# Kernel tuning notes

Hardware: AMD Instinct MI355X
Metric: run time of the kernel (lower is better)

The kernel has to match this reference:

```python
import jax, jax.numpy as jnp
import numpy as np

B, N, S = 256, 512, 32
D_ENT, D_KEY, D_IN, D_FUNC, D_TYPE, H = 256, 32, 1024, 256, 259, 32


def _init_linear(k, out_d, in_d):
    kw, kb = jax.random.split(k)
    bound = 1.0 / np.sqrt(in_d)
    W = jax.random.uniform(kw, (out_d, in_d), minval=-bound, maxval=bound, dtype=jnp.float32)
    b = jax.random.uniform(kb, (out_d,), minval=-bound, maxval=bound, dtype=jnp.float32)
    return W, b


def setup_inputs() -> dict:
    key = jax.random.key(0)
    ks = jax.random.split(key, 16)
    inp = {
        "embedding": jax.random.normal(ks[0], (B, D_IN), jnp.float32),
        "available_unit_type_mask": (jax.random.uniform(ks[1], (B, D_TYPE)) < 0.5).astype(jnp.float32),
        "available_units_mask": jnp.ones((B, N), jnp.float32),
        "entity_embedding": jax.random.normal(ks[2], (B, N, D_ENT), jnp.float32),
        "selected_units": jax.random.randint(ks[3], (B, S), 0, N, dtype=jnp.int32),
        "end_embedding": jax.random.uniform(ks[4], (1, D_KEY), minval=-1.0, maxval=1.0, dtype=jnp.float32) / np.sqrt(D_KEY),
    }
    inp["W_key"], inp["b_key"] = _init_linear(ks[5], D_KEY, D_ENT)
    inp["W_func"], inp["b_func"] = _init_linear(ks[6], D_FUNC, D_TYPE)
    inp["W_fc1"], inp["b_fc1"] = _init_linear(ks[7], D_FUNC, D_IN)
    inp["W_fc2"], inp["b_fc2"] = _init_linear(ks[8], D_KEY, D_FUNC)
    inp["W_embed"], inp["b_embed"] = _init_linear(ks[9], D_IN, D_KEY)
    inp["W_ih"], inp["b_ih"] = _init_linear(ks[10], 4 * H, D_KEY)
    inp["W_hh"], inp["b_hh"] = _init_linear(ks[11], 4 * H, H)
    return inp


def reference(embedding, available_unit_type_mask, available_units_mask, entity_embedding,
              selected_units, end_embedding, W_key, b_key, W_func, b_func, W_fc1, b_fc1,
              W_fc2, b_fc2, W_embed, b_embed, W_ih, b_ih, W_hh, b_hh):
    Bv, Nv, _ = entity_embedding.shape
    Sv = selected_units.shape[1]
    # keys for each entity + end-flag embedding appended -> [B, N+1, key_dim]
    key_t = jnp.einsum('bnd,kd->bnk', entity_embedding, W_key) + b_key
    end = jnp.broadcast_to(end_embedding[None, :, :], (Bv, 1, end_embedding.shape[1]))
    pad_key = jnp.concatenate([key_t, end], axis=1)
    # mask: entities + end flag; teacher-forced selected positions forced to 1
    mask0 = jnp.concatenate([available_units_mask, jnp.ones((Bv, 1), available_units_mask.dtype)], axis=1)
    mask0 = mask0.at[jnp.arange(Bv)[:, None], selected_units].set(1.0)
    func_embed = jax.nn.relu(available_unit_type_mask @ W_func.T + b_func)
    inv_n = 1.0 / jnp.float32(Nv)  # split_entity_num = end_flag_index = num_units
    bidx = jnp.arange(Bv)
    # per-step selected index (dummy 0 on the final end-flag step) and validity
    sel_seq = jnp.concatenate([selected_units.T, jnp.zeros((1, Bv), selected_units.dtype)], axis=0)
    valid_seq = jnp.concatenate([jnp.ones((Sv, Bv), jnp.float32), jnp.zeros((1, Bv), jnp.float32)], axis=0)

    def step(carry, xs):
        emb, h, c, mask = carry
        sel, valid = xs
        # query = fc2(relu(fc1(emb) + func_embed))
        x = jax.nn.relu(emb @ W_fc1.T + b_fc1 + func_embed) @ W_fc2.T + b_fc2
        # one LSTM step
        gates = x @ W_ih.T + b_ih + h @ W_hh.T + b_hh
        i_g, f_g, g_g, o_g = jnp.split(gates, 4, axis=1)
        c = jax.nn.sigmoid(f_g) * c + jax.nn.sigmoid(i_g) * jnp.tanh(g_g)
        h = jax.nn.sigmoid(o_g) * jnp.tanh(c)
        # masked dot-product over keys -> logits [B, N+1]
        q = jnp.einsum('bk,bnk->bn', h, pad_key) - (1.0 - mask) * 1e9
        # mark selected unit unavailable for subsequent steps
        mask = mask.at[bidx, sel].set(jnp.where(valid > 0, 0.0, mask[bidx, sel]))
        # one-hot gather of selected key, averaged, fed back into embedding
        emb_sel = pad_key[bidx, sel] * inv_n
        emb = emb + (emb_sel @ W_embed.T + b_embed) * valid[:, None]
        return (emb, h, c, mask), q

    h0 = jnp.zeros((Bv, W_hh.shape[1]), jnp.float32)
    c0 = jnp.zeros_like(h0)
    (emb, _, _, _), logits = jax.lax.scan(step, (embedding, h0, c0, mask0), (sel_seq, valid_seq))
    logits = jnp.transpose(logits, (1, 0, 2))  # [B, S+1, N+1]
    return logits, emb
```

## Files before the change

kernel.cpp:

```cpp
#include <hip/hip_runtime.h>
#include <math.h>

#define BB_ 256
#define NN_ 512
#define SS_ 32
#define NP1 513
#define SP1 33
#define D_IN 1024
#define D_TYPE 259
#define INV_N (1.0f/512.0f)

#define N_ACT 256
#define COMB_BASE 256
#define N_COMB 32
#define END_BID 288
#define KEY_BASE 289
#define N_KEY 2048
#define FRONT_GRID (KEY_BASE + N_KEY)

typedef short s16x4 __attribute__((ext_vector_type(4)));
typedef short s16x8 __attribute__((ext_vector_type(8)));
typedef float f32x4 __attribute__((ext_vector_type(4)));

#if defined(__has_builtin)
#if __has_builtin(__builtin_amdgcn_rcpf)
#define FRCP(x) __builtin_amdgcn_rcpf(x)
#else
#define FRCP(x) (1.0f / (x))
#endif
#else
#define FRCP(x) (1.0f / (x))
#endif

__device__ __forceinline__ float fsig(float x) { return FRCP(1.0f + __expf(-x)); }
__device__ __forceinline__ float ftanh(float x) { return fmaf(-2.0f, FRCP(1.0f + __expf(2.0f * x)), 1.0f); }
__device__ __forceinline__ short f2bf(float f) {
    unsigned u = __float_as_uint(f);
    unsigned r = (u + 0x7FFFu + ((u >> 16) & 1u)) >> 16;
    return (short)r;
}
__device__ __forceinline__ float bf2f(short s) {
    unsigned u = ((unsigned)(unsigned short)s) << 16;
    return __uint_as_float(u);
}

__global__ __launch_bounds__(256) void front_kernel(
    const float* __restrict__ ent, const float* __restrict__ Wk,
    const float* __restrict__ bk, const float* __restrict__ endv,
    const float* __restrict__ Wemb, const float* __restrict__ bemb,
    const float* __restrict__ Wfc1, const float* __restrict__ emb0,
    const float* __restrict__ bfc1, const float* __restrict__ atm,
    const float* __restrict__ Wf, const float* __restrict__ bf,
    short* __restrict__ pkbf, float* __restrict__ WcombT,
    float* __restrict__ cbv, float* __restrict__ act_pre)
{
    __shared__ __align__(128) char u_raw[65536];
    short* a_st   = (short*)u_raw;
    float* wemb_s = (float*)(u_raw + 18688);
    float* a_lds  = (float*)u_raw;
    float* w_lds  = (float*)(u_raw + 16640);

    const int tid = threadIdx.x;
    const int bid = blockIdx.x;
    const int lane = tid & 63, w = tid >> 6;
    const int nl = lane & 15, q = lane >> 4;

    if (bid >= KEY_BASE) {
        float* kb = (float*)u_raw;
        const size_t rowbase = (size_t)(bid - KEY_BASE) * 64;

#define KSTAGE(kc_) do {                                                          \
        _Pragma("unroll")                                                         \
        for (int p_ = 0; p_ < 4; p_++) {                                          \
            int flat_ = p_ * 256 + tid;                                           \
            int row_ = flat_ >> 4, u_ = flat_ & 15;                               \
            int gf4_ = (u_ & 8) | ((u_ ^ row_) & 7);                              \
            const float* src_ = ent + (((rowbase + (size_t)row_) << 8)            \
                                       + (kc_) * 64 + gf4_ * 4);                  \
            char* dst_ = u_raw + (kc_) * 16384 + ((p_ << 8) + (w << 6)) * 16;     \
            __builtin_amdgcn_global_load_lds(                                     \
                (const __attribute__((address_space(1))) void*)src_,              \
                (__attribute__((address_space(3))) void*)dst_, 16, 0, 0);         \
        }                                                                         \
    } while (0)

        KSTAGE(0);
        KSTAGE(1);
        KSTAGE(2);
        KSTAGE(3);

        s16x8 bfr[8][2];
#pragma unroll
        for (int s = 0; s < 8; s++)
#pragma unroll
            for (int t = 0; t < 2; t++) {
                const float* src = Wk + (size_t)(t * 16 + nl) * 256 + s * 32 + q * 8;
                float4 v0 = *(const float4*)(src);
                float4 v1 = *(const float4*)(src + 4);
                s16x8 bv;
                bv[0] = f2bf(v0.x); bv[1] = f2bf(v0.y); bv[2] = f2bf(v0.z); bv[3] = f2bf(v0.w);
                bv[4] = f2bf(v1.x); bv[5] = f2bf(v1.y); bv[6] = f2bf(v1.z); bv[7] = f2bf(v1.w);
                bfr[s][t] = bv;
            }

        f32x4 acc[2];
        acc[0] = (f32x4)0.0f; acc[1] = (f32x4)0.0f;

        const int rl = w * 16 + nl;
        const int rx = rl & 7;

#define KWAIT(n_) do {                                                            \
        asm volatile("s_waitcnt vmcnt(" #n_ ")" ::: "memory");                    \
        __builtin_amdgcn_s_barrier();                                             \
        asm volatile("" ::: "memory");                                            \
    } while (0)
#define KCOMPUTE(kc_) do {                                                        \
        const float* kbc = kb + (kc_) * 4096;                                     \
        _Pragma("unroll")                                                         \
        for (int ks = 0; ks < 2; ks++) {                                          \
            int s0 = ks * 8 + ((q * 2) ^ rx);                                     \
            int s1 = ks * 8 + ((q * 2 + 1) ^ rx);                                 \
            f32x4 a0 = *(const f32x4*)&kbc[rl * 64 + s0 * 4];                     \
            f32x4 a1 = *(const f32x4*)&kbc[rl * 64 + s1 * 4];                     \
            s16x8 af;                                                             \
            af[0] = f2bf(a0[0]); af[1] = f2bf(a0[1]);                             \
            af[2] = f2bf(a0[2]); af[3] = f2bf(a0[3]);                             \
            af[4] = f2bf(a1[0]); af[5] = f2bf(a1[1]);                             \
            af[6] = f2bf(a1[2]); af[7] = f2bf(a1[3]);                             \
            acc[0] = __builtin_amdgcn_mfma_f32_16x16x32_bf16(                     \
                af, bfr[(kc_) * 2 + ks][0], acc[0], 0, 0, 0);                     \
            acc[1] = __builtin_amdgcn_mfma_f32_16x16x32_bf16(                     \
                af, bfr[(kc_) * 2 + ks][1], acc[1], 0, 0, 0);                     \
        }                                                                         \
    } while (0)

        KWAIT(12); KCOMPUTE(0);
        KWAIT(8);  KCOMPUTE(1);
        KWAIT(4);  KCOMPUTE(2);
        KWAIT(0);  KCOMPUTE(3);

#undef KCOMPUTE
#undef KWAIT
#undef KSTAGE

        float bkv0 = bk[nl], bkv1 = bk[16 + nl];
#pragma unroll
        for (int t = 0; t < 2; t++)
#pragma unroll
            for (int r = 0; r < 4; r++) {
                int rowg = (int)rowbase + w * 16 + q * 4 + r;
                int b = rowg >> 9, n = rowg & 511;
                pkbf[((size_t)b * NP1 + n) * 32 + t * 16 + nl] =
                    f2bf(acc[t][r] + (t ? bkv1 : bkv0));
            }
    } else if (bid < N_ACT) {
        const int idx = bid;
        const int jt = idx & 15, bt = idx >> 4;
        const int bb = tid >> 4, jj = tid & 15;

#pragma unroll 4
        for (int r = 0; r < 16; r++) {
            a_lds[r * 260 + tid] = atm[(size_t)(bt * 16 + r) * D_TYPE + tid];
            w_lds[r * 260 + tid] = Wf[(size_t)(jt * 16 + r) * D_TYPE + tid];
            if (tid < 3) {
                a_lds[r * 260 + 256 + tid] = atm[(size_t)(bt * 16 + r) * D_TYPE + 256 + tid];
                w_lds[r * 260 + 256 + tid] = Wf[(size_t)(jt * 16 + r) * D_TYPE + 256 + tid];
            }
        }
        __syncthreads();
        float accf;
        {
            float f0 = 0.0f, f1 = 0.0f, f2 = 0.0f, f3 = 0.0f;
            const float4* ap = (const float4*)&a_lds[bb * 260];
            const float4* wp = (const float4*)&w_lds[jj * 260];
#pragma unroll 8
            for (int i4 = 0; i4 < 64; i4++) {
                float4 a = ap[i4]; float4 wv = wp[i4];
                f0 = fmaf(a.x, wv.x, f0); f1 = fmaf(a.y, wv.y, f1);
                f2 = fmaf(a.z, wv.z, f2); f3 = fmaf(a.w, wv.w, f3);
            }
            accf = (f0 + f1) + (f2 + f3);
            for (int i = 256; i < 259; i++) accf = fmaf(a_lds[bb * 260 + i], w_lds[jj * 260 + i], accf);
        }
        float c0 = 0.0f, c1 = 0.0f, c2 = 0.0f, c3 = 0.0f;
        for (int c = 0; c < 4; c++) {
            __syncthreads();
#pragma unroll
            for (int p = 0; p < 4; p++) {
                int l4 = p * 256 + tid;
                int r = l4 >> 6, k4 = l4 & 63;
                *(float4*)&a_lds[r * 260 + k4 * 4] =
                    *(const float4*)(emb0 + (size_t)(bt * 16 + r) * D_IN + c * 256 + k4 * 4);
                *(float4*)&w_lds[r * 260 + k4 * 4] =
                    *(const float4*)(Wfc1 + (size_t)(jt * 16 + r) * D_IN + c * 256 + k4 * 4);
            }
            __syncthreads();
#pragma unroll 8
            for (int k4 = 0; k4 < 64; k4++) {
                float4 a = *(const float4*)&a_lds[bb * 260 + k4 * 4];
                float4 wv = *(const float4*)&w_lds[jj * 260 + k4 * 4];
                c0 = fmaf(a.x, wv.x, c0); c1 = fmaf(a.y, wv.y, c1);
                c2 = fmaf(a.z, wv.z, c2); c3 = fmaf(a.w, wv.w, c3);
            }
        }
        float acc = (c0 + c1) + (c2 + c3);
        const int b = bt * 16 + bb, j = jt * 16 + jj;
        act_pre[b * 256 + j] = acc + bfc1[j] + fmaxf(accf + bf[j], 0.0f);
    } else if (bid < END_BID) {
        const int cb = bid - COMB_BASE;
        const int kc = cb >> 1;
        const int m0 = cb & 1;

#pragma unroll
        for (int p = 0; p < 8; p++) {
            int flat = p * 256 + tid;
            int row = flat >> 4;
            int f4 = flat & 15;
            float4 v = *(const float4*)(Wfc1 + (size_t)(m0 * 128 + row) * D_IN + kc * 64 + f4 * 4);
            s16x4 sv;
            sv[0] = f2bf(v.x); sv[1] = f2bf(v.y); sv[2] = f2bf(v.z); sv[3] = f2bf(v.w);
            *(s16x4*)&a_st[row * 72 + f4 * 4] = sv;
        }
        {
            int r = tid >> 2, c0 = tid & 3;
#pragma unroll
            for (int cc = 0; cc < 9; cc++) {
                int col = c0 + cc * 4;
                if (col < 33) {
                    float v = (col < 32) ? Wemb[(size_t)(kc * 64 + r) * 32 + col]
                                         : bemb[kc * 64 + r];
                    wemb_s[r * 33 + col] = v;
                }
            }
        }
        __syncthreads();

        f32x4 acc[2][3];
#pragma unroll
        for (int mt = 0; mt < 2; mt++)
#pragma unroll
            for (int t = 0; t < 3; t++) acc[mt][t] = (f32x4)0.0f;

#pragma unroll
        for (int ks = 0; ks < 2; ks++) {
            s16x8 bv[3];
#pragma unroll
            for (int t = 0; t < 3; t++) {
                int n = t * 16 + nl;
#pragma unroll
                for (int jj = 0; jj < 8; jj++) {
                    float v = (n < 33) ? wemb_s[(ks * 32 + q * 8 + jj) * 33 + n] : 0.0f;
                    bv[t][jj] = f2bf(v);
                }
            }
#pragma unroll
            for (int mt = 0; mt < 2; mt++) {
                s16x8 af = *(const s16x8*)&a_st[(w * 32 + mt * 16 + nl) * 72 + ks * 32 + q * 8];
#pragma unroll
                for (int t = 0; t < 3; t++)
                    acc[mt][t] = __builtin_amdgcn_mfma_f32_16x16x32_bf16(af, bv[t], acc[mt][t], 0, 0, 0);
            }
        }
#pragma unroll
        for (int mt = 0; mt < 2; mt++)
#pragma unroll
            for (int t = 0; t < 3; t++)
#pragma unroll
                for (int r = 0; r < 4; r++) {
                    int j = m0 * 128 + w * 32 + mt * 16 + q * 4 + r;
                    int n = t * 16 + nl;
                    if (n < 32) atomicAdd(&WcombT[j * 32 + n], acc[mt][t][r]);
                    else if (n == 32) atomicAdd(&cbv[j], acc[mt][t][r]);
                }
    } else {
        const int k = tid & 31, b0 = tid >> 5;
        short evk = f2bf(endv[k]);
        for (int b = b0; b < BB_; b += 8)
            pkbf[((size_t)b * NP1 + 512) * 32 + k] = evk;
    }
}

__global__ __launch_bounds__(512, 1) void back_kernel(
    const short* __restrict__ pkbf, const float* __restrict__ act_pre0,
    const int* __restrict__ sel, const float* __restrict__ avail,
    const float* __restrict__ Wfc2, const float* __restrict__ bfc2,
    const float* __restrict__ Wih, const float* __restrict__ bih,
    const float* __restrict__ bhh, const float* __restrict__ Whh,
    const float* __restrict__ WcombT, const float* __restrict__ cbv,
    const float* __restrict__ emb0, const float* __restrict__ Wemb,
    const float* __restrict__ bemb,
    float* __restrict__ logits, float* __restrict__ emb_out)
{
    __shared__ float S[19204];
    __shared__ int sel_l[SS_];
    float* rap_l  = S;
    float* red_l  = S + 8580;
    float* x_l    = S + 17028;
    float* cumE_l = S + 18084;
    float* ssel_l = S + 19140;
    float* xg_l   = S;
    float* h_all  = S + 4224;
    float* m0_l   = S + 8580;
    int*   tf_l   = (int*)(S + 9093);

    const int tid = threadIdx.x;
    const int b = blockIdx.x;
    const int lane = tid & 63, w = tid >> 6;
    const int nl = lane & 15, q = lane >> 4;

    if (tid < SS_) sel_l[tid] = sel[b * SS_ + tid];

    {
        const int k = tid & 31, sq = (tid >> 5) & 7;
        const int sq4 = sq * 4;
        int s0 = sel[b * SS_ + sq4 + 0];
        int s1 = sel[b * SS_ + sq4 + 1];
        int s2 = sel[b * SS_ + sq4 + 2];
        int s3 = sel[b * SS_ + sq4 + 3];
        float v0 = bf2f(pkbf[((size_t)b * NP1 + s0) * 32 + k]) * INV_N;
        float v1 = bf2f(pkbf[((size_t)b * NP1 + s1) * 32 + k]) * INV_N;
        float v2 = bf2f(pkbf[((size_t)b * NP1 + s2) * 32 + k]) * INV_N;
        float v3 = bf2f(pkbf[((size_t)b * NP1 + s3) * 32 + k]) * INV_N;
        float p0 = v0, p1 = p0 + v1, p2 = p1 + v2, p3 = p2 + v3;
        x_l[sq * 32 + k] = p3;
        __syncthreads();
        float off = 0.0f;
        for (int p = 0; p < 8; p++) if (p < sq) off += x_l[p * 32 + k];
        cumE_l[(sq4 + 1) * 32 + k] = off + p0;
        cumE_l[(sq4 + 2) * 32 + k] = off + p1;
        cumE_l[(sq4 + 3) * 32 + k] = off + p2;
        cumE_l[(sq4 + 4) * 32 + k] = off + p3;
        if (tid < 32) cumE_l[tid] = 0.0f;
        if (sq == 7) ssel_l[k] = off + p3;
    }
    __syncthreads();

    {
        const int j = tid & 255, half = tid >> 8;
        float wcr[32];
#pragma unroll
        for (int k4 = 0; k4 < 8; k4++) {
            float4 v = *(const float4*)(WcombT + (size_t)j * 32 + k4 * 4);
            wcr[k4*4] = v.x; wcr[k4*4+1] = v.y; wcr[k4*4+2] = v.z; wcr[k4*4+3] = v.w;
        }
        const float cbr = cbv[j];
        const float ap0v = act_pre0[b * 256 + j];
        for (int t = half; t < SP1; t += 2) {
            float ap = fmaf((float)t, cbr, ap0v), apb = 0.0f;
            const float4* ce = (const float4*)&cumE_l[t * 32];
#pragma unroll
            for (int k4 = 0; k4 < 8; k4++) {
                float4 e = ce[k4];
                ap  = fmaf(e.x, wcr[k4*4], ap);   apb = fmaf(e.y, wcr[k4*4+1], apb);
                ap  = fmaf(e.z, wcr[k4*4+2], ap); apb = fmaf(e.w, wcr[k4*4+3], apb);
            }
            rap_l[t * 260 + j] = fmaxf(ap + apb, 0.0f);
        }
    }
    __syncthreads();

    {
        const int i = tid & 31, seg = (tid >> 5) & 7, half = tid >> 8;
        float wfc2r[32];
#pragma unroll
        for (int i4 = 0; i4 < 8; i4++) {
            float4 v = *(const float4*)(Wfc2 + (size_t)i * 256 + seg * 32 + i4 * 4);
            wfc2r[i4*4] = v.x; wfc2r[i4*4+1] = v.y; wfc2r[i4*4+2] = v.z; wfc2r[i4*4+3] = v.w;
        }
        for (int t = half; t < SP1; t += 2) {
            float pa = 0.0f, pb = 0.0f;
            const float4* rp = (const float4*)&rap_l[t * 260 + seg * 32];
#pragma unroll
            for (int i4 = 0; i4 < 8; i4++) {
                float4 rv = rp[i4];
                pa = fmaf(rv.x, wfc2r[i4*4], pa);   pb = fmaf(rv.y, wfc2r[i4*4+1], pb);
                pa = fmaf(rv.z, wfc2r[i4*4+2], pa); pb = fmaf(rv.w, wfc2r[i4*4+3], pb);
            }
            red_l[t * 256 + seg * 32 + i] = pa + pb;
        }
    }
    __syncthreads();

    for (int p = 0; p < 3; p++) {
        int idx = p * 512 + tid;
        if (idx < SP1 * 32) {
            int t = idx >> 5, i = idx & 31;
            float x = bfc2[i];
#pragma unroll
            for (int s = 0; s < 8; s++) x += red_l[t * 256 + s * 32 + i];
            x_l[t * 32 + i] = x;
        }
    }
    __syncthreads();

    {
        const int g = tid & 127, qtr = tid >> 7;
        float wihr[32];
#pragma unroll
        for (int k4 = 0; k4 < 8; k4++) {
            float4 v = *(const float4*)(Wih + (size_t)g * 32 + k4 * 4);
            wihr[k4*4] = v.x; wihr[k4*4+1] = v.y; wihr[k4*4+2] = v.z; wihr[k4*4+3] = v.w;
        }
        const float bihg = bih[g] + bhh[g];
        for (int t = qtr; t < SP1; t += 4) {
            float ga = bihg, gb = 0.0f;
            const float4* xp = (const float4*)&x_l[t * 32];
#pragma unroll
            for (int k4 = 0; k4 < 8; k4++) {
                float4 xv = xp[k4];
                ga = fmaf(xv.x, wihr[k4*4], ga);   gb = fmaf(xv.y, wihr[k4*4+1], gb);
                ga = fmaf(xv.z, wihr[k4*4+2], ga); gb = fmaf(xv.w, wihr[k4*4+3], gb);
            }
            xg_l[t * 128 + g] = ga + gb;
        }
    }
    __syncthreads();

    if (tid < 64) {
        float whh0[32], whh1[32];
#pragma unroll
        for (int k4 = 0; k4 < 8; k4++) {
            float4 v0 = *(const float4*)(Whh + (size_t)tid * 32 + k4 * 4);
            float4 v1 = *(const float4*)(Whh + (size_t)(tid + 64) * 32 + k4 * 4);
            whh0[k4*4] = v0.x; whh0[k4*4+1] = v0.y; whh0[k4*4+2] = v0.z; whh0[k4*4+3] = v0.w;
            whh1[k4*4] = v1.x; whh1[k4*4+1] = v1.y; whh1[k4*4+2] = v1.z; whh1[k4*4+3] = v1.w;
        }
        float c = 0.0f;
        for (int t = 0; t < SP1; ++t) {
            float g0 = xg_l[t * 128 + tid];
            float g1 = xg_l[t * 128 + 64 + tid];
            if (t > 0) {
                float hv[32];
#pragma unroll
                for (int k4 = 0; k4 < 8; k4++) {
                    f32x4 v = *(const f32x4*)&h_all[(t - 1) * 32 + k4 * 4];
                    hv[k4*4] = v[0]; hv[k4*4+1] = v[1]; hv[k4*4+2] = v[2]; hv[k4*4+3] = v[3];
                }
                float g0a = 0.0f, g0b = 0.0f, g1a = 0.0f, g1b = 0.0f;
#pragma unroll
                for (int k = 0; k < 32; k += 2) {
                    g0a = fmaf(hv[k], whh0[k], g0a);     g0b = fmaf(hv[k+1], whh0[k+1], g0b);
                    g1a = fmaf(hv[k], whh1[k], g1a);     g1b = fmaf(hv[k+1], whh1[k+1], g1b);
                }
                g0 += g0a + g0b;
                g1 += g1a + g1b;
            }
            float og0 = __shfl_xor(g0, 32);
            float og1 = __shfl_xor(g1, 32);
            float ig = fsig(g0);
            float fg = fsig(og0);
            float gv = ftanh(g1);
            float og = fsig(og1);
            float cn = fg * c + ig * gv;
            float hn = og * ftanh(cn);
            if (tid < 32) {
                c = cn;
                h_all[t * 32 + tid] = hn;
            }
        }
    } else {
        for (int n = tid - 64; n < NP1; n += 448) {
            float m = (n < NN_) ? avail[(size_t)b * NN_ + n] : 1.0f;
            int tf = 1000;
#pragma unroll 8
            for (int s = 0; s < SS_; s++) {
                int sv = sel_l[s];
                if (sv == n) { m = 1.0f; if (s < tf) tf = s; }
            }
            m0_l[n] = m; tf_l[n] = tf;
        }
    }
    __syncthreads();

    {
        s16x8 afr[3];
#pragma unroll
        for (int mt = 0; mt < 3; mt++) {
            int row = mt * 16 + nl;
            s16x8 av;
#pragma unroll
            for (int jj = 0; jj < 8; jj++) {
                float v = (row < SP1) ? h_all[row * 32 + q * 8 + jj] : 0.0f;
                av[jj] = f2bf(v);
            }
            afr[mt] = av;
        }
        s16x8 bvr[5]; float m0v[5]; int tfv[5]; bool nvv[5];
#pragma unroll
        for (int ii = 0; ii < 5; ii++) {
            int tt = w + ii * 8;
            int n = tt * 16 + nl;
            bool nv = (tt < 33) && (n < NP1);
            nvv[ii] = nv;
            bvr[ii] = nv ? *(const s16x8*)(pkbf + ((size_t)b * NP1 + n) * 32 + q * 8) : (s16x8)0;
            m0v[ii] = nv ? m0_l[n] : 0.0f;
            tfv[ii] = nv ? tf_l[n] : 0;
        }
#pragma unroll
        for (int ii = 0; ii < 5; ii++) {
            int tt = w + ii * 8;
            if (tt >= 33) break;
            int n = tt * 16 + nl;
            f32x4 acc[3];
#pragma unroll
            for (int mt = 0; mt < 3; mt++)
                acc[mt] = __builtin_amdgcn_mfma_f32_16x16x32_bf16(afr[mt], bvr[ii], (f32x4)0.0f, 0, 0, 0);
#pragma unroll
            for (int mt = 0; mt < 3; mt++)
#pragma unroll
                for (int r = 0; r < 4; r++) {
                    int t = mt * 16 + q * 4 + r;
                    if (t < SP1 && nvv[ii]) {
                        float mv = (t <= tfv[ii]) ? m0v[ii] : 0.0f;
                        logits[((size_t)b * SP1 + t) * NP1 + n] = acc[mt][r] - (1.0f - mv) * 1e9f;
                    }
                }
        }
    }

#pragma unroll
    for (int p = 0; p < 2; p++) {
        int i = p * 512 + tid;
        float acca = emb0[(size_t)b * D_IN + i] + 32.0f * bemb[i];
        float accb = 0.0f;
        const float* wr = Wemb + (size_t)i * 32;
#pragma unroll
        for (int k4 = 0; k4 < 8; k4++) {
            float4 wv = *(const float4*)(wr + k4 * 4);
            acca = fmaf(ssel_l[k4*4+0], wv.x, acca);
            accb = fmaf(ssel_l[k4*4+1], wv.y, accb);
            acca = fmaf(ssel_l[k4*4+2], wv.z, acca);
            accb = fmaf(ssel_l[k4*4+3], wv.w, accb);
        }
        emb_out[(size_t)b * D_IN + i] = acca + accb;
    }
}

extern "C" void kernel_launch(void* const* d_in, const int* in_sizes, int n_in,
                              void* d_out, int out_size, void* d_ws, size_t ws_size,
                              hipStream_t stream)
{
    (void)in_sizes; (void)n_in; (void)out_size; (void)ws_size;
    const float* embedding = (const float*)d_in[0];
    const float* atm       = (const float*)d_in[1];
    const float* avail     = (const float*)d_in[2];
    const float* ent       = (const float*)d_in[3];
    const int*   sel       = (const int*)  d_in[4];
    const float* endv      = (const float*)d_in[5];
    const float* Wk   = (const float*)d_in[6];
    const float* bk   = (const float*)d_in[7];
    const float* Wf   = (const float*)d_in[8];
    const float* bf   = (const float*)d_in[9];
    const float* Wfc1 = (const float*)d_in[10];
    const float* bfc1 = (const float*)d_in[11];
    const float* Wfc2 = (const float*)d_in[12];
    const float* bfc2 = (const float*)d_in[13];
    const float* Wemb = (const float*)d_in[14];
    const float* bemb = (const float*)d_in[15];
    const float* Wih  = (const float*)d_in[16];
    const float* bih  = (const float*)d_in[17];
    const float* Whh  = (const float*)d_in[18];
    const float* bhh  = (const float*)d_in[19];

    float* ws = (float*)d_ws;
    float* act_pre = ws;
    float* WcombT  = act_pre + BB_ * 256;
    float* cbv     = WcombT + 256 * 32;
    short* pkbf    = (short*)(cbv + 256);

    float* logits  = (float*)d_out;
    float* emb_out = logits + (size_t)BB_ * SP1 * NP1;

    hipMemsetAsync(WcombT, 0, (size_t)(256 * 32 + 256) * sizeof(float), stream);

    front_kernel<<<FRONT_GRID, 256, 0, stream>>>(ent, Wk, bk, endv, Wemb, bemb,
                                                 Wfc1, embedding, bfc1, atm, Wf, bf,
                                                 pkbf, WcombT, cbv, act_pre);
    back_kernel<<<BB_, 512, 0, stream>>>(pkbf, act_pre, sel, avail,
                                         Wfc2, bfc2, Wih, bih, bhh, Whh,
                                         WcombT, cbv, embedding, Wemb, bemb,
                                         logits, emb_out);
}
```

Measured before the change: 284.7 us.

## Process four key row tiles per block with ring-buffered LDS staging

The key-projection blocks now each handle 256 entity rows (four 64-row tiles) instead of 64, shrinking that part of the front grid from 2048 blocks to 512. The converted bf16 W_key fragments and bias are loaded once per block and reused across tiles. A four-slot LDS ring keeps async global-to-LDS loads in flight while earlier chunks are computed. Key blocks are also reordered to come first in the grid. The cost is lower parallelism, more accumulator registers, and an extra barrier for each recycled slot.

```diff
diff --git a/kernel.cpp b/kernel.cpp
--- a/kernel.cpp
+++ b/kernel.cpp
@@ -10,13 +10,11 @@
 #define D_TYPE 259
 #define INV_N (1.0f/512.0f)
 
-#define N_ACT 256
-#define COMB_BASE 256
-#define N_COMB 32
-#define END_BID 288
-#define KEY_BASE 289
-#define N_KEY 2048
-#define FRONT_GRID (KEY_BASE + N_KEY)
+#define KEYS_N 512
+#define ACT_BASE 512
+#define COMB_BASE 768
+#define END_BID 800
+#define FRONT_GRID 801
 
 typedef short s16x4 __attribute__((ext_vector_type(4)));
 typedef short s16x8 __attribute__((ext_vector_type(8)));
@@ -65,29 +63,12 @@
     const int lane = tid & 63, w = tid >> 6;
     const int nl = lane & 15, q = lane >> 4;
 
-    if (bid >= KEY_BASE) {
+    if (bid < KEYS_N) {
         float* kb = (float*)u_raw;
-        const size_t rowbase = (size_t)(bid - KEY_BASE) * 64;
-
-#define KSTAGE(kc_) do {                                                          \
-        _Pragma("unroll")                                                         \
-        for (int p_ = 0; p_ < 4; p_++) {                                          \
-            int flat_ = p_ * 256 + tid;                                           \
-            int row_ = flat_ >> 4, u_ = flat_ & 15;                               \
-            int gf4_ = (u_ & 8) | ((u_ ^ row_) & 7);                              \
-            const float* src_ = ent + (((rowbase + (size_t)row_) << 8)            \
-                                       + (kc_) * 64 + gf4_ * 4);                  \
-            char* dst_ = u_raw + (kc_) * 16384 + ((p_ << 8) + (w << 6)) * 16;     \
-            __builtin_amdgcn_global_load_lds(                                     \
-                (const __attribute__((address_space(1))) void*)src_,              \
-                (__attribute__((address_space(3))) void*)dst_, 16, 0, 0);         \
-        }                                                                         \
-    } while (0)
-
-        KSTAGE(0);
-        KSTAGE(1);
-        KSTAGE(2);
-        KSTAGE(3);
+        const size_t blockrow = (size_t)bid * 256;
+
+        const int rl = w * 16 + nl;
+        const int rx = rl & 7;
 
         s16x8 bfr[8][2];
 #pragma unroll
@@ -102,20 +83,45 @@
                 bv[4] = f2bf(v1.x); bv[5] = f2bf(v1.y); bv[6] = f2bf(v1.z); bv[7] = f2bf(v1.w);
                 bfr[s][t] = bv;
             }
-
-        f32x4 acc[2];
-        acc[0] = (f32x4)0.0f; acc[1] = (f32x4)0.0f;
-
-        const int rl = w * 16 + nl;
-        const int rx = rl & 7;
-
-#define KWAIT(n_) do {                                                            \
+        float bkv0 = bk[nl], bkv1 = bk[16 + nl];
+#pragma unroll
+        for (int s = 0; s < 8; s++)
+#pragma unroll
+            for (int t = 0; t < 2; t++)
+                asm volatile("" :: "v"(bfr[s][t]) : "memory");
+        asm volatile("" :: "v"(bkv0), "v"(bkv1) : "memory");
+
+        f32x4 acc[4][2];
+#pragma unroll
+        for (int t = 0; t < 4; t++) { acc[t][0] = (f32x4)0.0f; acc[t][1] = (f32x4)0.0f; }
+
+#define KSTAGE(c_) do {                                                           \
+        _Pragma("unroll")                                                         \
+        for (int p_ = 0; p_ < 4; p_++) {                                          \
+            int flat_ = p_ * 256 + tid;                                           \
+            int row_ = flat_ >> 4, u_ = flat_ & 15;                               \
+            int gf4_ = (u_ & 8) | ((u_ ^ row_) & 7);                              \
+            const float* src_ = ent +                                             \
+                ((blockrow + ((c_) >> 2) * 64 + (size_t)row_) << 8)               \
+                + ((c_) & 3) * 64 + gf4_ * 4;                                     \
+            char* dst_ = u_raw + ((c_) & 3) * 16384 + ((p_ << 8) + (w << 6)) * 16;\
+            __builtin_amdgcn_global_load_lds(                                     \
+                (const __attribute__((address_space(1))) void*)src_,              \
+                (__attribute__((address_space(3))) void*)dst_, 16, 0, 0);         \
+        }                                                                         \
+    } while (0)
+#define KWAITB(n_) do {                                                           \
         asm volatile("s_waitcnt vmcnt(" #n_ ")" ::: "memory");                    \
         __builtin_amdgcn_s_barrier();                                             \
         asm volatile("" ::: "memory");                                            \
     } while (0)
-#define KCOMPUTE(kc_) do {                                                        \
-        const float* kbc = kb + (kc_) * 4096;                                     \
+#define KRECYC do {                                                               \
+        asm volatile("s_waitcnt lgkmcnt(0)" ::: "memory");                        \
+        __builtin_amdgcn_s_barrier();                                             \
+        asm volatile("" ::: "memory");                                            \
+    } while (0)
+#define KCOMPUTE(c_, t_) do {                                                     \
+        const float* kbc = kb + ((c_) & 3) * 4096;                                \
         _Pragma("unroll")                                                         \
         for (int ks = 0; ks < 2; ks++) {                                          \
             int s0 = ks * 8 + ((q * 2) ^ rx);                                     \
@@ -127,34 +133,48 @@
             af[2] = f2bf(a0[2]); af[3] = f2bf(a0[3]);                             \
             af[4] = f2bf(a1[0]); af[5] = f2bf(a1[1]);                             \
             af[6] = f2bf(a1[2]); af[7] = f2bf(a1[3]);                             \
-            acc[0] = __builtin_amdgcn_mfma_f32_16x16x32_bf16(                     \
-                af, bfr[(kc_) * 2 + ks][0], acc[0], 0, 0, 0);                     \
-            acc[1] = __builtin_amdgcn_mfma_f32_16x16x32_bf16(                     \
-                af, bfr[(kc_) * 2 + ks][1], acc[1], 0, 0, 0);                     \
+            acc[t_][0] = __builtin_amdgcn_mfma_f32_16x16x32_bf16(                 \
+                af, bfr[((c_) & 3) * 2 + ks][0], acc[t_][0], 0, 0, 0);            \
+            acc[t_][1] = __builtin_amdgcn_mfma_f32_16x16x32_bf16(                 \
+                af, bfr[((c_) & 3) * 2 + ks][1], acc[t_][1], 0, 0, 0);            \
         }                                                                         \
     } while (0)
 
-        KWAIT(12); KCOMPUTE(0);
-        KWAIT(8);  KCOMPUTE(1);
-        KWAIT(4);  KCOMPUTE(2);
-        KWAIT(0);  KCOMPUTE(3);
+        KSTAGE(0); KSTAGE(1); KSTAGE(2); KSTAGE(3);
+
+        KWAITB(12); KCOMPUTE(0, 0);  KRECYC; KSTAGE(4);
+        KWAITB(12); KCOMPUTE(1, 0);  KRECYC; KSTAGE(5);
+        KWAITB(12); KCOMPUTE(2, 0);  KRECYC; KSTAGE(6);
+        KWAITB(12); KCOMPUTE(3, 0);  KRECYC; KSTAGE(7);
+        KWAITB(12); KCOMPUTE(4, 1);  KRECYC; KSTAGE(8);
+        KWAITB(12); KCOMPUTE(5, 1);  KRECYC; KSTAGE(9);
+        KWAITB(12); KCOMPUTE(6, 1);  KRECYC; KSTAGE(10);
+        KWAITB(12); KCOMPUTE(7, 1);  KRECYC; KSTAGE(11);
+        KWAITB(12); KCOMPUTE(8, 2);  KRECYC; KSTAGE(12);
+        KWAITB(12); KCOMPUTE(9, 2);  KRECYC; KSTAGE(13);
+        KWAITB(12); KCOMPUTE(10, 2); KRECYC; KSTAGE(14);
+        KWAITB(12); KCOMPUTE(11, 2); KRECYC; KSTAGE(15);
+        KWAITB(12); KCOMPUTE(12, 3);
+        KWAITB(8);  KCOMPUTE(13, 3);
+        KWAITB(4);  KCOMPUTE(14, 3);
+        KWAITB(0);  KCOMPUTE(15, 3);
 
 #undef KCOMPUTE
-#undef KWAIT
+#undef KRECYC
+#undef KWAITB
 #undef KSTAGE
 
-        float bkv0 = bk[nl], bkv1 = bk[16 + nl];
-#pragma unroll
-        for (int t = 0; t < 2; t++)
+#pragma unroll
+        for (int tile = 0; tile < 4; tile++)
 #pragma unroll
             for (int r = 0; r < 4; r++) {
-                int rowg = (int)rowbase + w * 16 + q * 4 + r;
+                int rowg = (int)blockrow + tile * 64 + w * 16 + q * 4 + r;
                 int b = rowg >> 9, n = rowg & 511;
-                pkbf[((size_t)b * NP1 + n) * 32 + t * 16 + nl] =
-                    f2bf(acc[t][r] + (t ? bkv1 : bkv0));
-            }
-    } else if (bid < N_ACT) {
-        const int idx = bid;
+                pkbf[((size_t)b * NP1 + n) * 32 + nl]      = f2bf(acc[tile][0][r] + bkv0);
+                pkbf[((size_t)b * NP1 + n) * 32 + 16 + nl] = f2bf(acc[tile][1][r] + bkv1);
+            }
+    } else if (bid < COMB_BASE) {
+        const int idx = bid - ACT_BASE;
         const int jt = idx & 15, bt = idx >> 4;
         const int bb = tid >> 4, jj = tid & 15;
 
```

Measured after the change: 293.0 us. +2.9%, slower.
